# Kernel tuning notes

Hardware: AMD Instinct MI355X
Metric: run time of the kernel (lower is better)

## Reference

```python
import jax, jax.numpy as jnp
import numpy as np

N = 500_000      # nodes
E = 4_000_000    # directed edges
G = 16_384       # graphs
XD = 64          # num_node_features
ED = 16          # num_edge_features
INNER = 512      # inner_atom_dim (config)
DEPTH = 4


def _lin(k, fan_out, fan_in):
    kw, kb = jax.random.split(k)
    s = 1.0 / np.sqrt(fan_in)
    return (jax.random.uniform(kw, (fan_out, fan_in), jnp.float32, -s, s),
            jax.random.uniform(kb, (fan_out,), jnp.float32, -s, s))


def setup_inputs() -> dict:
    key = jax.random.key(0)
    ks = jax.random.split(key, 8)
    x = jax.random.normal(ks[0], (N, XD), jnp.float32)
    edge_index = jax.random.randint(ks[1], (2, E), 0, N, dtype=jnp.int32)
    edge_attr = jax.random.normal(ks[2], (E, ED), jnp.float32)
    batch = jnp.sort(jax.random.randint(ks[3], (N,), 0, G, dtype=jnp.int32))
    W_in_w, W_in_b = _lin(ks[4], XD, XD + ED)      # AtomBondConv.W_in
    W_out_w, W_out_b = _lin(ks[5], INNER, XD)      # MyNet.W_out
    lin1_w, lin1_b = _lin(ks[6], 50, INNER)
    lin2_w, lin2_b = _lin(ks[7], 1, 50)
    return dict(x=x, edge_attr=edge_attr,
                W_in_w=W_in_w, W_in_b=W_in_b, W_out_w=W_out_w, W_out_b=W_out_b,
                lin1_w=lin1_w, lin1_b=lin1_b, lin2_w=lin2_w, lin2_b=lin2_b,
                edge_index=edge_index, batch=batch,
                smiles=0, is_supervised=1, num_graphs=G)


def reference(x, edge_attr, W_in_w, W_in_b, W_out_w, W_out_b,
              lin1_w, lin1_b, lin2_w, lin2_b,
              edge_index, batch, smiles, is_supervised, num_graphs):
    # Dropout layers are identity in eval mode; is_supervised only picks dropout.
    src, dst = edge_index[0], edge_index[1]
    n = x.shape[0]

    def conv(x):
        # message = concat(x[src], edge_attr); self-loop message = concat(x, 0)
        # aggr='add' scatter to dst. Split the concat to avoid a [E, XD+ED] gather copy.
        agg_x = jax.ops.segment_sum(x[src], dst, num_segments=n) + x  # self loops
        agg_e = jax.ops.segment_sum(edge_attr, dst, num_segments=n)   # zeros for self loops
        agg = jnp.concatenate([agg_x, agg_e], axis=1)                 # [N, XD+ED]
        return agg @ W_in_w.T + W_in_b                                # [N, XD]

    fp = jnp.zeros((num_graphs, W_out_w.shape[0]), x.dtype)
    for i in range(DEPTH + 1):
        atom_fp = jax.nn.softmax(x @ W_out_w.T + W_out_b, axis=1)     # [N, INNER]
        fp = fp + jax.ops.segment_sum(atom_fp, batch, num_segments=num_graphs)
        if i < DEPTH:  # original applies conv on last iter too, but result is unused
            x = conv(x)

    hidden = fp @ lin1_w.T + lin1_b          # [G, 50]
    out = hidden @ lin2_w.T + lin2_b         # [G, 1]
    return jax.nn.sigmoid(out)
```

## Files before the change

### kernel.cpp

```cpp
#include <hip/hip_runtime.h>

typedef unsigned short u16;
typedef short bfx8 __attribute__((ext_vector_type(8)));
typedef float fx4 __attribute__((ext_vector_type(4)));

__device__ __forceinline__ float b2f(u16 u) {
    union { unsigned u; float f; } c; c.u = ((unsigned)u) << 16; return c.f;
}
__device__ __forceinline__ u16 f2b(float f) {
    union { float f; unsigned u; } c; c.f = f;
    unsigned x = c.u;
    unsigned r = x + 0x7FFFu + ((x >> 16) & 1u);
    return (u16)(r >> 16);
}
__device__ __forceinline__ float bpk_lo(unsigned p) {
    union { unsigned u; float f; } c; c.u = p << 16; return c.f;
}
__device__ __forceinline__ float bpk_hi(unsigned p) {
    union { unsigned u; float f; } c; c.u = p & 0xFFFF0000u; return c.f;
}

__global__ void k_cast(const float* __restrict__ xf, u16* __restrict__ xb, int n8) {
    int t = blockIdx.x * 256 + threadIdx.x;
    if (t >= n8) return;
    const float4* p = (const float4*)xf;
    float4 a = p[t * 2], b = p[t * 2 + 1];
    u16 o[8];
    o[0] = f2b(a.x); o[1] = f2b(a.y); o[2] = f2b(a.z); o[3] = f2b(a.w);
    o[4] = f2b(b.x); o[5] = f2b(b.y); o[6] = f2b(b.z); o[7] = f2b(b.w);
    ((uint4*)xb)[t] = *(uint4*)o;
}


__global__ void k_deg(const int* __restrict__ dst, int* __restrict__ rp, int E) {
    int e = blockIdx.x * 256 + threadIdx.x;
    if (e < E) atomicAdd(&rp[dst[e]], 1);
}

#define SCAN_T 256
#define SCAN_I 8
#define SCAN_CH 2048

__global__ void k_scanA(int* __restrict__ rp, int* __restrict__ bsum, int N) {
    __shared__ int s[SCAN_T];
    int base = blockIdx.x * SCAN_CH + threadIdx.x * SCAN_I;
    int v[SCAN_I]; int tot = 0;
    for (int i = 0; i < SCAN_I; i++) {
        int idx = base + i;
        int x = (idx < N) ? rp[idx] : 0;
        v[i] = tot; tot += x;
    }
    s[threadIdx.x] = tot; __syncthreads();
    for (int off = 1; off < SCAN_T; off <<= 1) {
        int t = (threadIdx.x >= off) ? s[threadIdx.x - off] : 0;
        __syncthreads();
        s[threadIdx.x] += t;
        __syncthreads();
    }
    int excl = (threadIdx.x == 0) ? 0 : s[threadIdx.x - 1];
    if (threadIdx.x == SCAN_T - 1) bsum[blockIdx.x] = s[SCAN_T - 1];
    for (int i = 0; i < SCAN_I; i++) {
        int idx = base + i;
        if (idx < N) rp[idx] = excl + v[i];
    }
}

__global__ void k_scanB(int* __restrict__ bsum, int nb) {
    __shared__ int s[SCAN_T];
    int t = threadIdx.x;
    s[t] = (t < nb) ? bsum[t] : 0; __syncthreads();
    for (int off = 1; off < SCAN_T; off <<= 1) {
        int v = (t >= off) ? s[t - off] : 0;
        __syncthreads();
        s[t] += v;
        __syncthreads();
    }
    if (t < nb) bsum[t] = (t == 0) ? 0 : s[t - 1];
}

__global__ void k_scanC(const int* __restrict__ bsum, int* __restrict__ rp,
                        int* __restrict__ cursor, int N, int E) {
    int i = blockIdx.x * 256 + threadIdx.x;
    if (i < N) {
        int v = rp[i] + bsum[i >> 11];
        rp[i] = v; cursor[i] = v;
    } else if (i == N) {
        rp[N] = E;
    }
}

__global__ void k_fill(const int* __restrict__ src, const int* __restrict__ dst,
                       int* __restrict__ cursor, int* __restrict__ col_src,
                       int* __restrict__ col_eid, int E) {
    int e = blockIdx.x * 256 + threadIdx.x;
    if (e >= E) return;
    int d = dst[e];
    int p = atomicAdd(&cursor[d], 1);
    col_src[p] = src[e];
    col_eid[p] = e;
}

__global__ void k_gptr(const int* __restrict__ batch, int* __restrict__ gptr, int N, int G) {
    int g = blockIdx.x * 256 + threadIdx.x;
    if (g > G) return;
    int lo = 0, hi = N;
    while (lo < hi) { int mid = (lo + hi) >> 1; if (batch[mid] < g) lo = mid + 1; else hi = mid; }
    gptr[g] = lo;
}

__global__ void k_agge(const float* __restrict__ ea, const int* __restrict__ rp,
                       const int* __restrict__ col_eid, float* __restrict__ agge, int N) {
    int t = blockIdx.x * 256 + threadIdx.x;
    int n = t >> 4, m = t & 15;
    if (n >= N) return;
    float v = 0.f;
    int p0 = rp[n], p1 = rp[n + 1];
    int last = p1 - 1;
    for (int p = p0; p < p1; p += 4) {
        int e[4];
#pragma unroll
        for (int k = 0; k < 4; k++) {
            int pk = p + k;
            e[k] = col_eid[pk < p1 ? pk : last];
        }
        float w[4];
#pragma unroll
        for (int k = 0; k < 4; k++) w[k] = ea[(size_t)e[k] * 16 + m];
#pragma unroll
        for (int k = 0; k < 4; k++) v += (p + k < p1) ? w[k] : 0.f;
    }
    agge[(size_t)n * 16 + m] = v;
}

__global__ __launch_bounds__(1024) void k_pass(
    const u16* __restrict__ x, const float* __restrict__ Wow, const float* __restrict__ Wob,
    const int* __restrict__ gptr, float* __restrict__ fp, int G, int writeMode)
{
    __shared__ u16 Wsw[64 * 64 * 8];
    for (int s = threadIdx.x; s < 4096; s += 1024) {
        int frag = s >> 6, lane = s & 63;
        int ft = frag >> 1, kt = frag & 1;
        int f = ft * 16 + (lane & 15);
        int k = kt * 32 + ((lane >> 4) & 3) * 8;
        const float* wp = Wow + f * 64 + k;
        u16 o[8];
#pragma unroll
        for (int i = 0; i < 8; i++) o[i] = f2b(wp[i]);
        ((uint4*)Wsw)[s] = *(uint4*)o;
    }
    __syncthreads();
    const int wid = threadIdx.x >> 6, lane = threadIdx.x & 63;
    const int quad = lane >> 4, col = lane & 15;

    unsigned bpk[16];
#pragma unroll
    for (int i = 0; i < 16; i++) {
        u16 lo = f2b(Wob[(2 * i) * 16 + col]);
        u16 hi = f2b(Wob[(2 * i + 1) * 16 + col]);
        bpk[i] = ((unsigned)lo) | (((unsigned)hi) << 16);
    }

    for (int g = blockIdx.x * 16 + wid; g < G; g += gridDim.x * 16) {
        int gs = gptr[g], ge = gptr[g + 1];
        int cnt = ge - gs;
        float fpacc[32];
#pragma unroll
        for (int t = 0; t < 32; t++) fpacc[t] = 0.f;

        for (int base = gs; base < ge; base += 32) {
            int n0 = base + col, n1 = base + 16 + col;
            bool v0 = n0 < ge, v1 = n1 < ge;
            const uint4* r0 = (const uint4*)(x + (size_t)(v0 ? n0 : gs) * 64);
            const uint4* r1 = (const uint4*)(x + (size_t)(v1 ? n1 : gs) * 64);
            uint4 a0u = r0[quad], a1u = r0[quad + 4];
            uint4 a2u = r1[quad], a3u = r1[quad + 4];
            if (!v0) { a0u.x = a0u.y = a0u.z = a0u.w = 0u; a1u = a0u; }
            if (!v1) { a2u.x = a2u.y = a2u.z = a2u.w = 0u; a3u = a2u; }
            bfx8 a0 = *(bfx8*)&a0u, a1 = *(bfx8*)&a1u;
            bfx8 a2 = *(bfx8*)&a2u, a3 = *(bfx8*)&a3u;

            float s0[4] = {0.f, 0.f, 0.f, 0.f}, s1[4] = {0.f, 0.f, 0.f, 0.f};
#pragma unroll 4
            for (int ft = 0; ft < 32; ft++) {
                float b = (ft & 1) ? bpk_hi(bpk[ft >> 1]) : bpk_lo(bpk[ft >> 1]);
                bfx8 b0 = *(bfx8*)(Wsw + ((ft * 2 + 0) * 64 + lane) * 8);
                bfx8 b1 = *(bfx8*)(Wsw + ((ft * 2 + 1) * 64 + lane) * 8);
                fx4 acc0 = {b, b, b, b}, acc1 = {b, b, b, b};
                acc0 = __builtin_amdgcn_mfma_f32_16x16x32_bf16(a0, b0, acc0, 0, 0, 0);
                acc0 = __builtin_amdgcn_mfma_f32_16x16x32_bf16(a1, b1, acc0, 0, 0, 0);
                acc1 = __builtin_amdgcn_mfma_f32_16x16x32_bf16(a2, b0, acc1, 0, 0, 0);
                acc1 = __builtin_amdgcn_mfma_f32_16x16x32_bf16(a3, b1, acc1, 0, 0, 0);
#pragma unroll
                for (int r = 0; r < 4; r++) {
                    s0[r] += __expf(acc0[r]);
                    s1[r] += __expf(acc1[r]);
                }
            }
            float rinv0[4], rinv1[4];
#pragma unroll
            for (int r = 0; r < 4; r++) {
                float t0 = s0[r], t1 = s1[r];
#pragma unroll
                for (int off = 1; off < 16; off <<= 1) {
                    t0 += __shfl_xor(t0, off, 64);
                    t1 += __shfl_xor(t1, off, 64);
                }
                int row0 = base - gs + quad * 4 + r;
                rinv0[r] = (row0 < cnt) ? __builtin_amdgcn_rcpf(t0) : 0.f;
                rinv1[r] = (row0 + 16 < cnt) ? __builtin_amdgcn_rcpf(t1) : 0.f;
            }
#pragma unroll 4
            for (int ft = 0; ft < 32; ft++) {
                float b = (ft & 1) ? bpk_hi(bpk[ft >> 1]) : bpk_lo(bpk[ft >> 1]);
                bfx8 b0 = *(bfx8*)(Wsw + ((ft * 2 + 0) * 64 + lane) * 8);
                bfx8 b1 = *(bfx8*)(Wsw + ((ft * 2 + 1) * 64 + lane) * 8);
                fx4 acc0 = {b, b, b, b}, acc1 = {b, b, b, b};
                acc0 = __builtin_amdgcn_mfma_f32_16x16x32_bf16(a0, b0, acc0, 0, 0, 0);
                acc0 = __builtin_amdgcn_mfma_f32_16x16x32_bf16(a1, b1, acc0, 0, 0, 0);
                acc1 = __builtin_amdgcn_mfma_f32_16x16x32_bf16(a2, b0, acc1, 0, 0, 0);
                acc1 = __builtin_amdgcn_mfma_f32_16x16x32_bf16(a3, b1, acc1, 0, 0, 0);
                float add = 0.f;
#pragma unroll
                for (int r = 0; r < 4; r++)
                    add += __expf(acc0[r]) * rinv0[r] + __expf(acc1[r]) * rinv1[r];
                fpacc[ft] += add;
            }
        }
#pragma unroll
        for (int ft = 0; ft < 32; ft++) {
            float v = fpacc[ft];
            v += __shfl_xor(v, 16, 64);
            v += __shfl_xor(v, 32, 64);
            if (lane < 16) {
                float* dp = fp + (size_t)g * 512 + ft * 16 + col;
                if (writeMode) *dp = v; else *dp += v;
            }
        }
    }
}

__global__ __launch_bounds__(256) void k_gemm(
    const u16* __restrict__ x, const float* __restrict__ Wiw, u16* __restrict__ y, int N)
{
    __shared__ u16 Wsw[8 * 64 * 8];
    for (int s = threadIdx.x; s < 512; s += 256) {
        int frag = s >> 6, lane = s & 63;
        int ft = frag >> 1, kt = frag & 1;
        int f = ft * 16 + (lane & 15);
        int k = kt * 32 + ((lane >> 4) & 3) * 8;
        const float* wp = Wiw + f * 80 + k;
        u16 o[8];
#pragma unroll
        for (int i = 0; i < 8; i++) o[i] = f2b(wp[i]);
        ((uint4*)Wsw)[s] = *(uint4*)o;
    }
    __syncthreads();
    const int wid = threadIdx.x >> 6, lane = threadIdx.x & 63;
    const int quad = lane >> 4, col = lane & 15;
    int ntile = N >> 4;
    for (int t = blockIdx.x * 4 + wid; t < ntile; t += gridDim.x * 4) {
        const uint4* rowp = (const uint4*)(x + (size_t)(t * 16 + col) * 64);
        uint4 a0u = rowp[quad], a1u = rowp[quad + 4];
        bfx8 a0 = *(bfx8*)&a0u, a1 = *(bfx8*)&a1u;
#pragma unroll
        for (int ft = 0; ft < 4; ft++) {
            fx4 acc = {0.f, 0.f, 0.f, 0.f};
            bfx8 b0 = *(bfx8*)(Wsw + ((ft * 2 + 0) * 64 + lane) * 8);
            bfx8 b1 = *(bfx8*)(Wsw + ((ft * 2 + 1) * 64 + lane) * 8);
            acc = __builtin_amdgcn_mfma_f32_16x16x32_bf16(a0, b0, acc, 0, 0, 0);
            acc = __builtin_amdgcn_mfma_f32_16x16x32_bf16(a1, b1, acc, 0, 0, 0);
#pragma unroll
            for (int r = 0; r < 4; r++)
                y[(size_t)(t * 16 + quad * 4 + r) * 64 + ft * 16 + col] = f2b(acc[r]);
        }
    }
}

__global__ __launch_bounds__(256) void k_gath(
    const u16* __restrict__ y, const float* __restrict__ agge,
    const float* __restrict__ Wiw, const float* __restrict__ Wib,
    const int* __restrict__ rp, const int* __restrict__ col_src,
    u16* __restrict__ xb, int N)
{
    __shared__ float W2t[16 * 64];
    __shared__ float bias[64];
    for (int s = threadIdx.x; s < 1024; s += 256) {
        int m = s >> 6, j = s & 63;
        W2t[s] = Wiw[j * 80 + 64 + m];
    }
    if (threadIdx.x < 64) bias[threadIdx.x] = Wib[threadIdx.x];
    __syncthreads();
    const int wid = threadIdx.x >> 6, lane = threadIdx.x & 63;
    const int half = lane >> 5, f = lane & 31;
    const int P = (N + 1) >> 1;
    const int nw = gridDim.x * 4;
    for (int i = blockIdx.x * 4 + wid; i < P; i += nw) {
        int n = i * 2 + half;
        bool valid = n < N;
        int nn = valid ? n : (N - 1);
        unsigned su = *(const unsigned*)(y + (size_t)nn * 64 + 2 * f);
        float ax = bpk_lo(su) + bias[2 * f];
        float ay = bpk_hi(su) + bias[2 * f + 1];
        int p0 = rp[nn], p1 = rp[nn + 1];
        int last = p1 - 1;
        for (int p = p0; p < p1; p += 8) {
            int s[8];
#pragma unroll
            for (int k = 0; k < 8; k++) {
                int pk = p + k;
                s[k] = col_src[pk < p1 ? pk : last];
            }
            unsigned u[8];
#pragma unroll
            for (int k = 0; k < 8; k++)
                u[k] = *(const unsigned*)(y + (size_t)s[k] * 64 + 2 * f);
            float sx = 0.f, sy = 0.f;
#pragma unroll
            for (int k = 0; k < 8; k++) {
                bool ok = (p + k) < p1;
                sx += ok ? bpk_lo(u[k]) : 0.f;
                sy += ok ? bpk_hi(u[k]) : 0.f;
            }
            ax += sx; ay += sy;
        }
        const float4* aev = (const float4*)(agge + (size_t)nn * 16);
#pragma unroll
        for (int q = 0; q < 4; q++) {
            float4 a4 = aev[q];
            int m0 = q * 4;
            ax += a4.x * W2t[(m0 + 0) * 64 + 2 * f] + a4.y * W2t[(m0 + 1) * 64 + 2 * f]
                + a4.z * W2t[(m0 + 2) * 64 + 2 * f] + a4.w * W2t[(m0 + 3) * 64 + 2 * f];
            ay += a4.x * W2t[(m0 + 0) * 64 + 2 * f + 1] + a4.y * W2t[(m0 + 1) * 64 + 2 * f + 1]
                + a4.z * W2t[(m0 + 2) * 64 + 2 * f + 1] + a4.w * W2t[(m0 + 3) * 64 + 2 * f + 1];
        }
        if (valid) {
            unsigned o = ((unsigned)f2b(ax)) | (((unsigned)f2b(ay)) << 16);
            *(unsigned*)(xb + (size_t)n * 64 + 2 * f) = o;
        }
    }
}

__global__ __launch_bounds__(256) void k_head(
    const float* __restrict__ fp, const float* __restrict__ l1w, const float* __restrict__ l1b,
    const float* __restrict__ l2w, const float* __restrict__ l2b, float* __restrict__ out, int G)
{
    const int wid = threadIdx.x >> 6, lane = threadIdx.x & 63;
    int g = blockIdx.x * 4 + wid;
    if (g >= G) return;
    int j = lane < 50 ? lane : 49;
    float h = 0.f;
    const float4* fv = (const float4*)(fp + (size_t)g * 512);
    const float4* wv = (const float4*)(l1w + (size_t)j * 512);
    for (int q = 0; q < 128; q++) {
        float4 w = wv[q], f = fv[q];
        h += w.x * f.x + w.y * f.y + w.z * f.z + w.w * f.w;
    }
    h += l1b[j];
    float val = (lane < 50) ? h * l2w[lane] : 0.f;
#pragma unroll
    for (int off = 1; off < 64; off <<= 1) val += __shfl_xor(val, off, 64);
    if (lane == 0) {
        float o = val + l2b[0];
        out[g] = 1.f / (1.f + __expf(-o));
    }
}

extern "C" void kernel_launch(void* const* d_in, const int* in_sizes, int n_in,
                              void* d_out, int out_size, void* d_ws, size_t ws_size,
                              hipStream_t stream)
{
    const float* x    = (const float*)d_in[0];
    const float* ea   = (const float*)d_in[1];
    const float* Wiw  = (const float*)d_in[2];
    const float* Wib  = (const float*)d_in[3];
    const float* Wow  = (const float*)d_in[4];
    const float* Wob  = (const float*)d_in[5];
    const float* l1w  = (const float*)d_in[6];
    const float* l1b  = (const float*)d_in[7];
    const float* l2w  = (const float*)d_in[8];
    const float* l2b  = (const float*)d_in[9];
    const int* ei     = (const int*)d_in[10];
    const int* batch  = (const int*)d_in[11];
    float* out = (float*)d_out;

    const int N = in_sizes[0] / 64;
    const int E = in_sizes[10] / 2;
    const int G = 16384;
    const int* src = ei;
    const int* dst = ei + E;

    size_t o = 0;
    auto give = [&](size_t bytes) {
        char* p = (char*)d_ws + o;
        o += (bytes + 255) & ~(size_t)255;
        return (void*)p;
    };
    u16*   x16     = (u16*)  give((size_t)N * 64 * 2);
    u16*   xb      = (u16*)  give((size_t)N * 64 * 2);
    u16*   y       = (u16*)  give((size_t)N * 64 * 2);
    float* agge    = (float*)give((size_t)N * 16 * 4);
    float* fp      = (float*)give((size_t)G * 512 * 4);
    int*   rp      = (int*)  give((size_t)(N + 1) * 4);
    int*   cursor  = (int*)  give((size_t)N * 4);
    int*   col_src = (int*)  give((size_t)E * 4);
    int*   col_eid = (int*)  give((size_t)E * 4);
    int*   bsum    = (int*)  give(4096);
    int*   gptr    = (int*)  give((size_t)(G + 1) * 4);

    hipMemsetAsync(rp, 0, (size_t)(N + 1) * 4, stream);
    k_deg<<<(E + 255) / 256, 256, 0, stream>>>(dst, rp, E);
    int nb = (N + SCAN_CH - 1) / SCAN_CH;
    k_scanA<<<nb, SCAN_T, 0, stream>>>(rp, bsum, N);
    k_scanB<<<1, SCAN_T, 0, stream>>>(bsum, nb);
    k_scanC<<<(N + 256) / 256, 256, 0, stream>>>(bsum, rp, cursor, N, E);
    k_fill<<<(E + 255) / 256, 256, 0, stream>>>(src, dst, cursor, col_src, col_eid, E);
    k_gptr<<<(G + 256) / 256, 256, 0, stream>>>(batch, gptr, N, G);
    k_agge<<<(N * 16 + 255) / 256, 256, 0, stream>>>(ea, rp, col_eid, agge, N);

    k_cast<<<(N * 64 / 8 + 255) / 256, 256, 0, stream>>>(x, x16, N * 64 / 8);

    k_pass<<<512, 1024, 0, stream>>>(x16, Wow, Wob, gptr, fp, G, 1);
    const u16* xc = x16;
    for (int d = 0; d < 4; d++) {
        k_gemm<<<1024, 256, 0, stream>>>(xc, Wiw, y, N);
        k_gath<<<2048, 256, 0, stream>>>(y, agge, Wiw, Wib, rp, col_src, xb, N);
        xc = xb;
        k_pass<<<512, 1024, 0, stream>>>(xc, Wow, Wob, gptr, fp, G, 0);
    }
    k_head<<<G / 4, 256, 0, stream>>>(fp, l1w, l1b, l2w, l2b, out, G);
}
```

Measured before the change: 2.780 ms.

## Restructure softmax pooling to one graph per block with LDS exp staging

k_pass now gives each block one graph and each wave two fixed 16-feature tiles with weights held in registers. The MFMA and exp for each 32-row chunk are computed once and written to LDS; row sums and the per-feature accumulation then run across the whole block. This replaces the old per-wave scheme, which recomputed all 512 logits and exps twice, and it prefetches the next chunk of node rows. Separately, col_src and col_eid are interleaved into one int2 array, which makes k_gath read 8-byte entries when it needs only 4 bytes. The new k_pass also adds three block-wide barriers per chunk and about 66KB of LDS, which can lower occupancy.

After: 3.418 ms. +22.9%, slower.

```diff
diff --git a/kernel.cpp b/kernel.cpp
--- a/kernel.cpp
+++ b/kernel.cpp
@@ -90,14 +90,12 @@
 }
 
 __global__ void k_fill(const int* __restrict__ src, const int* __restrict__ dst,
-                       int* __restrict__ cursor, int* __restrict__ col_src,
-                       int* __restrict__ col_eid, int E) {
+                       int* __restrict__ cursor, int2* __restrict__ col, int E) {
     int e = blockIdx.x * 256 + threadIdx.x;
     if (e >= E) return;
     int d = dst[e];
     int p = atomicAdd(&cursor[d], 1);
-    col_src[p] = src[e];
-    col_eid[p] = e;
+    col[p] = make_int2(src[e], e);
 }
 
 __global__ void k_gptr(const int* __restrict__ batch, int* __restrict__ gptr, int N, int G) {
@@ -109,7 +107,7 @@
 }
 
 __global__ void k_agge(const float* __restrict__ ea, const int* __restrict__ rp,
-                       const int* __restrict__ col_eid, float* __restrict__ agge, int N) {
+                       const int2* __restrict__ col, float* __restrict__ agge, int N) {
     int t = blockIdx.x * 256 + threadIdx.x;
     int n = t >> 4, m = t & 15;
     if (n >= N) return;
@@ -121,7 +119,7 @@
 #pragma unroll
         for (int k = 0; k < 4; k++) {
             int pk = p + k;
-            e[k] = col_eid[pk < p1 ? pk : last];
+            e[k] = col[pk < p1 ? pk : last].y;
         }
         float w[4];
 #pragma unroll
@@ -132,110 +130,101 @@
     agge[(size_t)n * 16 + m] = v;
 }
 
+#define EXP_STRIDE 516
 __global__ __launch_bounds__(1024) void k_pass(
     const u16* __restrict__ x, const float* __restrict__ Wow, const float* __restrict__ Wob,
     const int* __restrict__ gptr, float* __restrict__ fp, int G, int writeMode)
 {
-    __shared__ u16 Wsw[64 * 64 * 8];
-    for (int s = threadIdx.x; s < 4096; s += 1024) {
-        int frag = s >> 6, lane = s & 63;
-        int ft = frag >> 1, kt = frag & 1;
-        int f = ft * 16 + (lane & 15);
-        int k = kt * 32 + ((lane >> 4) & 3) * 8;
+    __shared__ float expL[32 * EXP_STRIDE];
+    __shared__ float rinvL[32];
+    __shared__ float combL[512];
+
+    const int tid = threadIdx.x;
+    const int wid = tid >> 6, lane = tid & 63;
+    const int quad = lane >> 4, col = lane & 15;
+    const int ft0 = wid * 2, ft1 = ft0 + 1;
+
+    bfx8 B[4];
+#pragma unroll
+    for (int i = 0; i < 4; i++) {
+        int ft = (i >> 1) ? ft1 : ft0, kt = i & 1;
+        int f = ft * 16 + col;
+        int k = kt * 32 + quad * 8;
         const float* wp = Wow + f * 64 + k;
         u16 o[8];
 #pragma unroll
-        for (int i = 0; i < 8; i++) o[i] = f2b(wp[i]);
-        ((uint4*)Wsw)[s] = *(uint4*)o;
-    }
-    __syncthreads();
-    const int wid = threadIdx.x >> 6, lane = threadIdx.x & 63;
-    const int quad = lane >> 4, col = lane & 15;
-
-    unsigned bpk[16];
-#pragma unroll
-    for (int i = 0; i < 16; i++) {
-        u16 lo = f2b(Wob[(2 * i) * 16 + col]);
-        u16 hi = f2b(Wob[(2 * i + 1) * 16 + col]);
-        bpk[i] = ((unsigned)lo) | (((unsigned)hi) << 16);
-    }
-
-    for (int g = blockIdx.x * 16 + wid; g < G; g += gridDim.x * 16) {
-        int gs = gptr[g], ge = gptr[g + 1];
-        int cnt = ge - gs;
-        float fpacc[32];
-#pragma unroll
-        for (int t = 0; t < 32; t++) fpacc[t] = 0.f;
+        for (int j = 0; j < 8; j++) o[j] = f2b(wp[j]);
+        B[i] = *(bfx8*)o;
+    }
+    const float bias0 = Wob[ft0 * 16 + col], bias1 = Wob[ft1 * 16 + col];
+
+    const int fC = tid & 511, hC = tid >> 9;
+    const int tn = tid >> 5, tc = tid & 31;
+
+    for (int g = blockIdx.x; g < G; g += gridDim.x) {
+        const int gs = gptr[g], ge = gptr[g + 1];
+        float fpacc = 0.f;
+
+        uint4 f0, f1, f2, f3;
+        {
+            int b = gs;
+            if (b < ge) {
+                int n0 = b + col, n1 = n0 + 16;
+                const uint4* r0 = (const uint4*)(x + (size_t)((n0 < ge) ? n0 : gs) * 64);
+                const uint4* r1 = (const uint4*)(x + (size_t)((n1 < ge) ? n1 : gs) * 64);
+                f0 = r0[quad]; f1 = r0[quad + 4]; f2 = r1[quad]; f3 = r1[quad + 4];
+            }
+        }
 
         for (int base = gs; base < ge; base += 32) {
-            int n0 = base + col, n1 = base + 16 + col;
-            bool v0 = n0 < ge, v1 = n1 < ge;
-            const uint4* r0 = (const uint4*)(x + (size_t)(v0 ? n0 : gs) * 64);
-            const uint4* r1 = (const uint4*)(x + (size_t)(v1 ? n1 : gs) * 64);
-            uint4 a0u = r0[quad], a1u = r0[quad + 4];
-            uint4 a2u = r1[quad], a3u = r1[quad + 4];
-            if (!v0) { a0u.x = a0u.y = a0u.z = a0u.w = 0u; a1u = a0u; }
-            if (!v1) { a2u.x = a2u.y = a2u.z = a2u.w = 0u; a3u = a2u; }
-            bfx8 a0 = *(bfx8*)&a0u, a1 = *(bfx8*)&a1u;
-            bfx8 a2 = *(bfx8*)&a2u, a3 = *(bfx8*)&a3u;
-
-            float s0[4] = {0.f, 0.f, 0.f, 0.f}, s1[4] = {0.f, 0.f, 0.f, 0.f};
-#pragma unroll 4
-            for (int ft = 0; ft < 32; ft++) {
-                float b = (ft & 1) ? bpk_hi(bpk[ft >> 1]) : bpk_lo(bpk[ft >> 1]);
-                bfx8 b0 = *(bfx8*)(Wsw + ((ft * 2 + 0) * 64 + lane) * 8);
-                bfx8 b1 = *(bfx8*)(Wsw + ((ft * 2 + 1) * 64 + lane) * 8);
-                fx4 acc0 = {b, b, b, b}, acc1 = {b, b, b, b};
-                acc0 = __builtin_amdgcn_mfma_f32_16x16x32_bf16(a0, b0, acc0, 0, 0, 0);
-                acc0 = __builtin_amdgcn_mfma_f32_16x16x32_bf16(a1, b1, acc0, 0, 0, 0);
-                acc1 = __builtin_amdgcn_mfma_f32_16x16x32_bf16(a2, b0, acc1, 0, 0, 0);
-                acc1 = __builtin_amdgcn_mfma_f32_16x16x32_bf16(a3, b1, acc1, 0, 0, 0);
-#pragma unroll
-                for (int r = 0; r < 4; r++) {
-                    s0[r] += __expf(acc0[r]);
-                    s1[r] += __expf(acc1[r]);
-                }
+            int rows = ge - base; if (rows > 32) rows = 32;
+            bfx8 a0 = *(bfx8*)&f0, a1 = *(bfx8*)&f1, a2 = *(bfx8*)&f2, a3 = *(bfx8*)&f3;
+            if (base + 32 < ge) {
+                int b = base + 32;
+                int n0 = b + col, n1 = n0 + 16;
+                const uint4* r0 = (const uint4*)(x + (size_t)((n0 < ge) ? n0 : gs) * 64);
+                const uint4* r1 = (const uint4*)(x + (size_t)((n1 < ge) ? n1 : gs) * 64);
+                f0 = r0[quad]; f1 = r0[quad + 4]; f2 = r1[quad]; f3 = r1[quad + 4];
             }
-            float rinv0[4], rinv1[4];
+            fx4 c00 = {bias0, bias0, bias0, bias0}, c01 = c00;
+            fx4 c10 = {bias1, bias1, bias1, bias1}, c11 = c10;
+            c00 = __builtin_amdgcn_mfma_f32_16x16x32_bf16(a0, B[0], c00, 0, 0, 0);
+            c00 = __builtin_amdgcn_mfma_f32_16x16x32_bf16(a1, B[1], c00, 0, 0, 0);
+            c01 = __builtin_amdgcn_mfma_f32_16x16x32_bf16(a2, B[0], c01, 0, 0, 0);
+            c01 = __builtin_amdgcn_mfma_f32_16x16x32_bf16(a3, B[1], c01, 0, 0, 0);
+            c10 = __builtin_amdgcn_mfma_f32_16x16x32_bf16(a0, B[2], c10, 0, 0, 0);
+            c10 = __builtin_amdgcn_mfma_f32_16x16x32_bf16(a1, B[3], c10, 0, 0, 0);
+            c11 = __builtin_amdgcn_mfma_f32_16x16x32_bf16(a2, B[2], c11, 0, 0, 0);
+            c11 = __builtin_amdgcn_mfma_f32_16x16x32_bf16(a3, B[3], c11, 0, 0, 0);
 #pragma unroll
             for (int r = 0; r < 4; r++) {
-                float t0 = s0[r], t1 = s1[r];
-#pragma unroll
-                for (int off = 1; off < 16; off <<= 1) {
-                    t0 += __shfl_xor(t0, off, 64);
-                    t1 += __shfl_xor(t1, off, 64);
-                }
-                int row0 = base - gs + quad * 4 + r;
-                rinv0[r] = (row0 < cnt) ? __builtin_amdgcn_rcpf(t0) : 0.f;
-                rinv1[r] = (row0 + 16 < cnt) ? __builtin_amdgcn_rcpf(t1) : 0.f;
+                int row0 = quad * 4 + r;
+                expL[row0 * EXP_STRIDE + ft0 * 16 + col]        = __expf(c00[r]);
+                expL[(row0 + 16) * EXP_STRIDE + ft0 * 16 + col] = __expf(c01[r]);
+                expL[row0 * EXP_STRIDE + ft1 * 16 + col]        = __expf(c10[r]);
+                expL[(row0 + 16) * EXP_STRIDE + ft1 * 16 + col] = __expf(c11[r]);
             }
-#pragma unroll 4
-            for (int ft = 0; ft < 32; ft++) {
-                float b = (ft & 1) ? bpk_hi(bpk[ft >> 1]) : bpk_lo(bpk[ft >> 1]);
-                bfx8 b0 = *(bfx8*)(Wsw + ((ft * 2 + 0) * 64 + lane) * 8);
-                bfx8 b1 = *(bfx8*)(Wsw + ((ft * 2 + 1) * 64 + lane) * 8);
-                fx4 acc0 = {b, b, b, b}, acc1 = {b, b, b, b};
-                acc0 = __builtin_amdgcn_mfma_f32_16x16x32_bf16(a0, b0, acc0, 0, 0, 0);
-                acc0 = __builtin_amdgcn_mfma_f32_16x16x32_bf16(a1, b1, acc0, 0, 0, 0);
-                acc1 = __builtin_amdgcn_mfma_f32_16x16x32_bf16(a2, b0, acc1, 0, 0, 0);
-                acc1 = __builtin_amdgcn_mfma_f32_16x16x32_bf16(a3, b1, acc1, 0, 0, 0);
-                float add = 0.f;
-#pragma unroll
-                for (int r = 0; r < 4; r++)
-                    add += __expf(acc0[r]) * rinv0[r] + __expf(acc1[r]) * rinv1[r];
-                fpacc[ft] += add;
-            }
-        }
-#pragma unroll
-        for (int ft = 0; ft < 32; ft++) {
-            float v = fpacc[ft];
-            v += __shfl_xor(v, 16, 64);
-            v += __shfl_xor(v, 32, 64);
-            if (lane < 16) {
-                float* dp = fp + (size_t)g * 512 + ft * 16 + col;
-                if (writeMode) *dp = v; else *dp += v;
-            }
-        }
+            __syncthreads();
+            float part = 0.f;
+            int rb = tn * EXP_STRIDE + tc;
+#pragma unroll
+            for (int j = 0; j < 16; j++) part += expL[rb + j * 32];
+#pragma unroll
+            for (int off = 1; off < 32; off <<= 1) part += __shfl_xor(part, off, 64);
+            if (tc == 0) rinvL[tn] = (tn < rows) ? __builtin_amdgcn_rcpf(part) : 0.f;
+            __syncthreads();
+            for (int n = hC; n < rows; n += 2)
+                fpacc += expL[n * EXP_STRIDE + fC] * rinvL[n];
+            __syncthreads();
+        }
+        if (hC == 1) combL[fC] = fpacc;
+        __syncthreads();
+        if (hC == 0) {
+            float v = fpacc + combL[fC];
+            float* dp = fp + (size_t)g * 512 + fC;
+            if (writeMode) *dp = v; else *dp += v;
+        }
+        __syncthreads();
     }
 }
 
@@ -279,7 +268,7 @@
 __global__ __launch_bounds__(256) void k_gath(
     const u16* __restrict__ y, const float* __restrict__ agge,
     const float* __restrict__ Wiw, const float* __restrict__ Wib,
-    const int* __restrict__ rp, const int* __restrict__ col_src,
+    const int* __restrict__ rp, const int2* __restrict__ col,
     u16* __restrict__ xb, int N)
 {
     __shared__ float W2t[16 * 64];
@@ -308,7 +297,7 @@
 #pragma unroll
             for (int k = 0; k < 8; k++) {
                 int pk = p + k;
-                s[k] = col_src[pk < p1 ? pk : last];
+                s[k] = col[pk < p1 ? pk : last].x;
             }
             unsigned u[8];
 #pragma unroll
@@ -402,8 +391,7 @@
     float* fp      = (float*)give((size_t)G * 512 * 4);
     int*   rp      = (int*)  give((size_t)(N + 1) * 4);
     int*   cursor  = (int*)  give((size_t)N * 4);
-    int*   col_src = (int*)  give((size_t)E * 4);
-    int*   col_eid = (int*)  give((size_t)E * 4);
+    int2*  col     = (int2*) give((size_t)E * 8);
     int*   bsum    = (int*)  give(4096);
     int*   gptr    = (int*)  give((size_t)(G + 1) * 4);
 
@@ -413,9 +401,9 @@
     k_scanA<<<nb, SCAN_T, 0, stream>>>(rp, bsum, N);
     k_scanB<<<1, SCAN_T, 0, stream>>>(bsum, nb);
     k_scanC<<<(N + 256) / 256, 256, 0, stream>>>(bsum, rp, cursor, N, E);
-    k_fill<<<(E + 255) / 256, 256, 0, stream>>>(src, dst, cursor, col_src, col_eid, E);
+    k_fill<<<(E + 255) / 256, 256, 0, stream>>>(src, dst, cursor, col, E);
     k_gptr<<<(G + 256) / 256, 256, 0, stream>>>(batch, gptr, N, G);
-    k_agge<<<(N * 16 + 255) / 256, 256, 0, stream>>>(ea, rp, col_eid, agge, N);
+    k_agge<<<(N * 16 + 255) / 256, 256, 0, stream>>>(ea, rp, col, agge, N);
 
     k_cast<<<(N * 64 / 8 + 255) / 256, 256, 0, stream>>>(x, x16, N * 64 / 8);
 
@@ -423,7 +411,7 @@
     const u16* xc = x16;
     for (int d = 0; d < 4; d++) {
         k_gemm<<<1024, 256, 0, stream>>>(xc, Wiw, y, N);
-        k_gath<<<2048, 256, 0, stream>>>(y, agge, Wiw, Wib, rp, col_src, xb, N);
+        k_gath<<<2048, 256, 0, stream>>>(y, agge, Wiw, Wib, rp, col, xb, N);
         xc = xb;
         k_pass<<<512, 1024, 0, stream>>>(xc, Wow, Wob, gptr, fp, G, 0);
     }
```

## Cache softmax exponentials in registers instead of recomputing MFMA pass

Applied to the files above, without the earlier changes.

The fingerprint kernel no longer runs the matmul and exp a second time for normalisation. It stores the exponentials as packed bf16 in 128 registers and reuses them after the row sums are known. It also prefetches the next node tile, reads the bias from LDS, and moves to 256-thread blocks with 2 blocks per CU. Separately, the CSR source and edge-id arrays are interleaved into one int2 array. The register-heavy epk array risks spills or low occupancy, and the exponentials lose precision by being rounded to bf16.

New measurement: 2.912 ms. 1.05x slower.

```diff
diff --git a/kernel.cpp b/kernel.cpp
--- a/kernel.cpp
+++ b/kernel.cpp
@@ -18,6 +18,11 @@
 }
 __device__ __forceinline__ float bpk_hi(unsigned p) {
     union { unsigned u; float f; } c; c.u = p & 0xFFFF0000u; return c.f;
+}
+__device__ __forceinline__ unsigned cvtpk(float lo, float hi) {
+    unsigned r;
+    asm("v_cvt_pk_bf16_f32 %0, %1, %2" : "=v"(r) : "v"(lo), "v"(hi));
+    return r;
 }
 
 __global__ void k_cast(const float* __restrict__ xf, u16* __restrict__ xb, int n8) {
@@ -90,14 +95,12 @@
 }
 
 __global__ void k_fill(const int* __restrict__ src, const int* __restrict__ dst,
-                       int* __restrict__ cursor, int* __restrict__ col_src,
-                       int* __restrict__ col_eid, int E) {
+                       int* __restrict__ cursor, int2* __restrict__ col, int E) {
     int e = blockIdx.x * 256 + threadIdx.x;
     if (e >= E) return;
     int d = dst[e];
     int p = atomicAdd(&cursor[d], 1);
-    col_src[p] = src[e];
-    col_eid[p] = e;
+    col[p] = make_int2(src[e], e);
 }
 
 __global__ void k_gptr(const int* __restrict__ batch, int* __restrict__ gptr, int N, int G) {
@@ -109,7 +112,7 @@
 }
 
 __global__ void k_agge(const float* __restrict__ ea, const int* __restrict__ rp,
-                       const int* __restrict__ col_eid, float* __restrict__ agge, int N) {
+                       const int2* __restrict__ col, float* __restrict__ agge, int N) {
     int t = blockIdx.x * 256 + threadIdx.x;
     int n = t >> 4, m = t & 15;
     if (n >= N) return;
@@ -121,7 +124,7 @@
 #pragma unroll
         for (int k = 0; k < 4; k++) {
             int pk = p + k;
-            e[k] = col_eid[pk < p1 ? pk : last];
+            e[k] = col[pk < p1 ? pk : last].y;
         }
         float w[4];
 #pragma unroll
@@ -132,12 +135,13 @@
     agge[(size_t)n * 16 + m] = v;
 }
 
-__global__ __launch_bounds__(1024) void k_pass(
+__global__ __launch_bounds__(256, 2) void k_pass(
     const u16* __restrict__ x, const float* __restrict__ Wow, const float* __restrict__ Wob,
     const int* __restrict__ gptr, float* __restrict__ fp, int G, int writeMode)
 {
     __shared__ u16 Wsw[64 * 64 * 8];
-    for (int s = threadIdx.x; s < 4096; s += 1024) {
+    __shared__ float biasL[512];
+    for (int s = threadIdx.x; s < 4096; s += 256) {
         int frag = s >> 6, lane = s & 63;
         int ft = frag >> 1, kt = frag & 1;
         int f = ft * 16 + (lane & 15);
@@ -148,41 +152,41 @@
         for (int i = 0; i < 8; i++) o[i] = f2b(wp[i]);
         ((uint4*)Wsw)[s] = *(uint4*)o;
     }
+    for (int s = threadIdx.x; s < 512; s += 256) biasL[s] = Wob[s];
     __syncthreads();
     const int wid = threadIdx.x >> 6, lane = threadIdx.x & 63;
     const int quad = lane >> 4, col = lane & 15;
 
-    unsigned bpk[16];
-#pragma unroll
-    for (int i = 0; i < 16; i++) {
-        u16 lo = f2b(Wob[(2 * i) * 16 + col]);
-        u16 hi = f2b(Wob[(2 * i + 1) * 16 + col]);
-        bpk[i] = ((unsigned)lo) | (((unsigned)hi) << 16);
-    }
-
-    for (int g = blockIdx.x * 16 + wid; g < G; g += gridDim.x * 16) {
-        int gs = gptr[g], ge = gptr[g + 1];
-        int cnt = ge - gs;
+    for (int g = blockIdx.x * 4 + wid; g < G; g += gridDim.x * 4) {
+        const int gs = gptr[g], ge = gptr[g + 1];
+        const int cnt = ge - gs;
         float fpacc[32];
 #pragma unroll
         for (int t = 0; t < 32; t++) fpacc[t] = 0.f;
 
+        uint4 p0, p1, p2, p3;
+        if (gs < ge) {
+            int n0 = gs + col, n1 = n0 + 16;
+            const uint4* r0 = (const uint4*)(x + (size_t)((n0 < ge) ? n0 : gs) * 64);
+            const uint4* r1 = (const uint4*)(x + (size_t)((n1 < ge) ? n1 : gs) * 64);
+            p0 = r0[quad]; p1 = r0[quad + 4]; p2 = r1[quad]; p3 = r1[quad + 4];
+        }
+
         for (int base = gs; base < ge; base += 32) {
-            int n0 = base + col, n1 = base + 16 + col;
-            bool v0 = n0 < ge, v1 = n1 < ge;
-            const uint4* r0 = (const uint4*)(x + (size_t)(v0 ? n0 : gs) * 64);
-            const uint4* r1 = (const uint4*)(x + (size_t)(v1 ? n1 : gs) * 64);
-            uint4 a0u = r0[quad], a1u = r0[quad + 4];
-            uint4 a2u = r1[quad], a3u = r1[quad + 4];
-            if (!v0) { a0u.x = a0u.y = a0u.z = a0u.w = 0u; a1u = a0u; }
-            if (!v1) { a2u.x = a2u.y = a2u.z = a2u.w = 0u; a3u = a2u; }
-            bfx8 a0 = *(bfx8*)&a0u, a1 = *(bfx8*)&a1u;
-            bfx8 a2 = *(bfx8*)&a2u, a3 = *(bfx8*)&a3u;
-
+            bfx8 a0 = *(bfx8*)&p0, a1 = *(bfx8*)&p1, a2 = *(bfx8*)&p2, a3 = *(bfx8*)&p3;
+            if (base + 32 < ge) {
+                int b = base + 32;
+                int n0 = b + col, n1 = n0 + 16;
+                const uint4* r0 = (const uint4*)(x + (size_t)((n0 < ge) ? n0 : gs) * 64);
+                const uint4* r1 = (const uint4*)(x + (size_t)((n1 < ge) ? n1 : gs) * 64);
+                p0 = r0[quad]; p1 = r0[quad + 4]; p2 = r1[quad]; p3 = r1[quad + 4];
+            }
+
+            unsigned epk[128];
             float s0[4] = {0.f, 0.f, 0.f, 0.f}, s1[4] = {0.f, 0.f, 0.f, 0.f};
-#pragma unroll 4
+#pragma unroll
             for (int ft = 0; ft < 32; ft++) {
-                float b = (ft & 1) ? bpk_hi(bpk[ft >> 1]) : bpk_lo(bpk[ft >> 1]);
+                float b = biasL[ft * 16 + col];
                 bfx8 b0 = *(bfx8*)(Wsw + ((ft * 2 + 0) * 64 + lane) * 8);
                 bfx8 b1 = *(bfx8*)(Wsw + ((ft * 2 + 1) * 64 + lane) * 8);
                 fx4 acc0 = {b, b, b, b}, acc1 = {b, b, b, b};
@@ -190,11 +194,16 @@
                 acc0 = __builtin_amdgcn_mfma_f32_16x16x32_bf16(a1, b1, acc0, 0, 0, 0);
                 acc1 = __builtin_amdgcn_mfma_f32_16x16x32_bf16(a2, b0, acc1, 0, 0, 0);
                 acc1 = __builtin_amdgcn_mfma_f32_16x16x32_bf16(a3, b1, acc1, 0, 0, 0);
-#pragma unroll
-                for (int r = 0; r < 4; r++) {
-                    s0[r] += __expf(acc0[r]);
-                    s1[r] += __expf(acc1[r]);
-                }
+                float e00 = __expf(acc0[0]), e01 = __expf(acc0[1]);
+                float e02 = __expf(acc0[2]), e03 = __expf(acc0[3]);
+                float e10 = __expf(acc1[0]), e11 = __expf(acc1[1]);
+                float e12 = __expf(acc1[2]), e13 = __expf(acc1[3]);
+                s0[0] += e00; s0[1] += e01; s0[2] += e02; s0[3] += e03;
+                s1[0] += e10; s1[1] += e11; s1[2] += e12; s1[3] += e13;
+                epk[ft * 4 + 0] = cvtpk(e00, e01);
+                epk[ft * 4 + 1] = cvtpk(e02, e03);
+                epk[ft * 4 + 2] = cvtpk(e10, e11);
+                epk[ft * 4 + 3] = cvtpk(e12, e13);
             }
             float rinv0[4], rinv1[4];
 #pragma unroll
@@ -209,20 +218,13 @@
                 rinv0[r] = (row0 < cnt) ? __builtin_amdgcn_rcpf(t0) : 0.f;
                 rinv1[r] = (row0 + 16 < cnt) ? __builtin_amdgcn_rcpf(t1) : 0.f;
             }
-#pragma unroll 4
+#pragma unroll
             for (int ft = 0; ft < 32; ft++) {
-                float b = (ft & 1) ? bpk_hi(bpk[ft >> 1]) : bpk_lo(bpk[ft >> 1]);
-                bfx8 b0 = *(bfx8*)(Wsw + ((ft * 2 + 0) * 64 + lane) * 8);
-                bfx8 b1 = *(bfx8*)(Wsw + ((ft * 2 + 1) * 64 + lane) * 8);
-                fx4 acc0 = {b, b, b, b}, acc1 = {b, b, b, b};
-                acc0 = __builtin_amdgcn_mfma_f32_16x16x32_bf16(a0, b0, acc0, 0, 0, 0);
-                acc0 = __builtin_amdgcn_mfma_f32_16x16x32_bf16(a1, b1, acc0, 0, 0, 0);
-                acc1 = __builtin_amdgcn_mfma_f32_16x16x32_bf16(a2, b0, acc1, 0, 0, 0);
-                acc1 = __builtin_amdgcn_mfma_f32_16x16x32_bf16(a3, b1, acc1, 0, 0, 0);
-                float add = 0.f;
-#pragma unroll
-                for (int r = 0; r < 4; r++)
-                    add += __expf(acc0[r]) * rinv0[r] + __expf(acc1[r]) * rinv1[r];
+                float add =
+                      bpk_lo(epk[ft * 4 + 0]) * rinv0[0] + bpk_hi(epk[ft * 4 + 0]) * rinv0[1]
+                    + bpk_lo(epk[ft * 4 + 1]) * rinv0[2] + bpk_hi(epk[ft * 4 + 1]) * rinv0[3]
+                    + bpk_lo(epk[ft * 4 + 2]) * rinv1[0] + bpk_hi(epk[ft * 4 + 2]) * rinv1[1]
+                    + bpk_lo(epk[ft * 4 + 3]) * rinv1[2] + bpk_hi(epk[ft * 4 + 3]) * rinv1[3];
                 fpacc[ft] += add;
             }
         }
@@ -279,7 +281,7 @@
 __global__ __launch_bounds__(256) void k_gath(
     const u16* __restrict__ y, const float* __restrict__ agge,
     const float* __restrict__ Wiw, const float* __restrict__ Wib,
-    const int* __restrict__ rp, const int* __restrict__ col_src,
+    const int* __restrict__ rp, const int2* __restrict__ col,
     u16* __restrict__ xb, int N)
 {
     __shared__ float W2t[16 * 64];
@@ -308,7 +310,7 @@
 #pragma unroll
             for (int k = 0; k < 8; k++) {
                 int pk = p + k;
-                s[k] = col_src[pk < p1 ? pk : last];
+                s[k] = col[pk < p1 ? pk : last].x;
             }
             unsigned u[8];
 #pragma unroll
@@ -402,8 +404,7 @@
     float* fp      = (float*)give((size_t)G * 512 * 4);
     int*   rp      = (int*)  give((size_t)(N + 1) * 4);
     int*   cursor  = (int*)  give((size_t)N * 4);
-    int*   col_src = (int*)  give((size_t)E * 4);
-    int*   col_eid = (int*)  give((size_t)E * 4);
+    int2*  col     = (int2*) give((size_t)E * 8);
     int*   bsum    = (int*)  give(4096);
     int*   gptr    = (int*)  give((size_t)(G + 1) * 4);
 
@@ -413,19 +414,19 @@
     k_scanA<<<nb, SCAN_T, 0, stream>>>(rp, bsum, N);
     k_scanB<<<1, SCAN_T, 0, stream>>>(bsum, nb);
     k_scanC<<<(N + 256) / 256, 256, 0, stream>>>(bsum, rp, cursor, N, E);
-    k_fill<<<(E + 255) / 256, 256, 0, stream>>>(src, dst, cursor, col_src, col_eid, E);
+    k_fill<<<(E + 255) / 256, 256, 0, stream>>>(src, dst, cursor, col, E);
     k_gptr<<<(G + 256) / 256, 256, 0, stream>>>(batch, gptr, N, G);
-    k_agge<<<(N * 16 + 255) / 256, 256, 0, stream>>>(ea, rp, col_eid, agge, N);
+    k_agge<<<(N * 16 + 255) / 256, 256, 0, stream>>>(ea, rp, col, agge, N);
 
     k_cast<<<(N * 64 / 8 + 255) / 256, 256, 0, stream>>>(x, x16, N * 64 / 8);
 
-    k_pass<<<512, 1024, 0, stream>>>(x16, Wow, Wob, gptr, fp, G, 1);
+    k_pass<<<2048, 256, 0, stream>>>(x16, Wow, Wob, gptr, fp, G, 1);
     const u16* xc = x16;
     for (int d = 0; d < 4; d++) {
         k_gemm<<<1024, 256, 0, stream>>>(xc, Wiw, y, N);
-        k_gath<<<2048, 256, 0, stream>>>(y, agge, Wiw, Wib, rp, col_src, xb, N);
+        k_gath<<<2048, 256, 0, stream>>>(y, agge, Wiw, Wib, rp, col, xb, N);
         xc = xb;
-        k_pass<<<512, 1024, 0, stream>>>(xc, Wow, Wob, gptr, fp, G, 0);
+        k_pass<<<2048, 256, 0, stream>>>(xc, Wow, Wob, gptr, fp, G, 0);
     }
     k_head<<<G / 4, 256, 0, stream>>>(fp, l1w, l1b, l2w, l2b, out, G);
 }
```
